# Optimization experiments

Measured on AMD Instinct MI355X. Metric: run time of the kernel, lower is better.

## Reference

```python
import jax, jax.numpy as jnp
import numpy as np

B, S = 256, 512
V, E, H, O = 256, 128, 256, 128


def setup_inputs() -> dict:
    key = jax.random.key(0)
    ks = jax.random.split(key, 8)
    s_e = 1.0 / np.sqrt(H)
    return {
        "x": jax.random.randint(ks[0], (B, S), 0, V),
        "emb": jax.random.normal(ks[1], (V, E), dtype=jnp.float32),
        "W_ih": jax.random.uniform(ks[2], (4 * H, E), jnp.float32, -s_e, s_e),
        "W_hh": jax.random.uniform(ks[3], (4 * H, H), jnp.float32, -s_e, s_e),
        "b_ih": jax.random.uniform(ks[4], (4 * H,), jnp.float32, -s_e, s_e),
        "b_hh": jax.random.uniform(ks[5], (4 * H,), jnp.float32, -s_e, s_e),
        "W_out": jax.random.uniform(ks[6], (O, H), jnp.float32, -s_e, s_e),
        "b_out": jax.random.uniform(ks[7], (O,), jnp.float32, -s_e, s_e),
    }


def _lstm_last_h(xe, W_ih, W_hh, b_ih, b_hh):
    # xe: [B, S, E]. Precompute input contribution to all gates: [S, B, 4H]
    pre = jnp.einsum("bse,ge->sbg", xe, W_ih) + (b_ih + b_hh)
    Bn = xe.shape[0]
    h0 = jnp.zeros((Bn, H), xe.dtype)
    c0 = jnp.zeros((Bn, H), xe.dtype)

    def step(carry, p):
        h, c = carry
        gates = p + h @ W_hh.T  # [B, 4H]
        i, f, g, o = jnp.split(gates, 4, axis=-1)  # PyTorch gate order i,f,g,o
        i = jax.nn.sigmoid(i)
        f = jax.nn.sigmoid(f)
        g = jnp.tanh(g)
        o = jax.nn.sigmoid(o)
        c = f * c + i * g
        h = o * jnp.tanh(c)
        return (h, c), None

    (h, _), _ = jax.lax.scan(step, (h0, c0), pre)
    return h  # [B, H] == lstm output at last timestep


def reference(x, emb, W_ih, W_hh, b_ih, b_hh, W_out, b_out):
    xe = emb[x]  # [B, S, E] embedding lookup
    h_last = _lstm_last_h(xe, W_ih, W_hh, b_ih, b_hh)
    return h_last @ W_out.T + b_out  # [B, O]
```

## Files before the change

kernel.cpp:

```cpp
#include <hip/hip_runtime.h>


typedef _Float16 f16x8 __attribute__((ext_vector_type(8)));
typedef _Float16 f16x4 __attribute__((ext_vector_type(4)));
typedef float    f32x4 __attribute__((ext_vector_type(4)));

#define B_  256
#define S_  512
#define V_  256
#define E_  128
#define H_  256
#define O_  128

#define T_OFF     0u
#define HLAST_OFF (512u << 10)
#define WPK_OFF   (768u << 10)

__global__ void build_table(const float* __restrict__ emb,
                            const float* __restrict__ W_ih,
                            const float* __restrict__ b_ih,
                            const float* __restrict__ b_hh,
                            _Float16* __restrict__ T2h) {
    const int v   = blockIdx.x;
    const int tid = threadIdx.x;

    __shared__ float e[E_];
    if (tid < E_) e[tid] = emb[v * E_ + tid];
    __syncthreads();

    f16x4 tv;
#pragma unroll
    for (int t = 0; t < 4; ++t) {
        const int g = t * 256 + tid;
        const float4* wp = (const float4*)(W_ih + g * E_);
        float acc = 0.f;
#pragma unroll
        for (int i = 0; i < E_ / 4; ++i) {
            float4 w = wp[i];
            acc += w.x * e[4*i] + w.y * e[4*i+1] + w.z * e[4*i+2] + w.w * e[4*i+3];
        }
        tv[t] = (_Float16)(acc + b_ih[g] + b_hh[g]);
    }
    *(f16x4*)(T2h + ((size_t)v * 256 + tid) * 4) = tv;
}

__global__ void prepack(const float* __restrict__ W_hh,
                        _Float16* __restrict__ Wpk) {
    const int blk = blockIdx.x;
    const int ktS = blk >> 3;
    const int j   = blk & 7;
    const int kt  = 3 + ktS * 4;
    const int tid = threadIdx.x;
    const int wv = tid >> 6, l = tid & 63, l15 = l & 15, quad = l >> 4;
    const int n  = j * 128 + wv * 16 + l15;
    const int k0 = kt * 32 + quad * 8;
    const float4* wp = (const float4*)(W_hh + (size_t)n * H_ + k0);
    float4 w0 = wp[0];
    float4 w1 = wp[1];
    f16x8 f = (f16x8){
        (_Float16)w0.x, (_Float16)w0.y, (_Float16)w0.z, (_Float16)w0.w,
        (_Float16)w1.x, (_Float16)w1.y, (_Float16)w1.z, (_Float16)w1.w};
    *(f16x8*)(Wpk + ((size_t)tid * 16 + blk) * 8) = f;
}

__device__ __forceinline__ float sig_fast(float x) {
    float t = __builtin_amdgcn_exp2f(-1.4426950408889634f * x);
    return __builtin_amdgcn_rcpf(1.f + t);
}
__device__ __forceinline__ float tanh_fast(float x) {
    x = fminf(fmaxf(x, -30.f), 30.f);
    float t = __builtin_amdgcn_exp2f(-2.8853900817779268f * x);
    return (1.f - t) * __builtin_amdgcn_rcpf(1.f + t);
}

#define HSTRIDE 272

__launch_bounds__(512, 2)
__global__ void lstm_persistent(const int* __restrict__ x,
                                const float* __restrict__ W_hh,
                                const _Float16* __restrict__ T2h,
                                const _Float16* __restrict__ Wpk,
                                float* __restrict__ hlast) {
    const int tid    = threadIdx.x;
    const int wv     = tid >> 6;
    const int l      = tid & 63;
    const int l15    = l & 15;
    const int quad   = l >> 4;
    const int stripe = blockIdx.x;
    const int uu     = wv * 16 + l15;

    __shared__ __align__(16) _Float16 wlds[8][8][2][512];
    __shared__ __align__(16) _Float16 hbuf[2][4][HSTRIDE];
    __shared__ __align__(16) _Float16 zbuf[256];

    if (tid < 128) ((int*)zbuf)[tid] = 0;

    f16x8 wreg[8][4];
#pragma unroll
    for (int j = 0; j < 8; ++j) {
        const float* wr = W_hh + (size_t)(j * 128 + uu) * H_ + quad * 8;
#pragma unroll
        for (int kt = 0; kt < 7; ++kt) {
            if (kt == 3) continue;
            const float4* wp = (const float4*)(wr + kt * 32);
            float4 w0 = wp[0];
            float4 w1 = wp[1];
            f16x8 f = (f16x8){
                (_Float16)w0.x, (_Float16)w0.y, (_Float16)w0.z, (_Float16)w0.w,
                (_Float16)w1.x, (_Float16)w1.y, (_Float16)w1.z, (_Float16)w1.w};
            if (kt < 2)
                *(f16x8*)&wlds[wv][j][kt][(size_t)l * 8] = f;
            else
                wreg[j][(kt == 2) ? 0 : kt - 3] = f;
        }
    }

    const int grow = stripe * 4 + quad;
    float c2[2] = {0.f, 0.f};

    const int* xp = x + (size_t)grow * S_;
    int xv = xp[0];

    f16x8 wstr[8];
    const _Float16* wpk_lane = Wpk + (size_t)tid * 128;

    const f32x4 z4 = (f32x4){0.f, 0.f, 0.f, 0.f};

    __syncthreads();

    for (int s = 0; s < S_; ++s) {
        f16x4 tcv[2];
        tcv[0] = *(const f16x4*)(T2h + ((size_t)xv * 256 + uu) * 4);
        tcv[1] = *(const f16x4*)(T2h + ((size_t)xv * 256 + uu + 128) * 4);
        if (s + 1 < S_) xv = xp[s + 1];

        f32x4 acc[8];

        if (s > 0) {
            const _Float16* ha = ((l15 & 3) == 0)
                ? (&hbuf[(s - 1) & 1][l15 >> 2][0] + quad * 8)
                : (zbuf + quad * 8);

            {
                f16x8 a = *(const f16x8*)(ha + 0 * 32);
#pragma unroll
                for (int j = 0; j < 8; ++j) {
                    f16x8 b = *(const f16x8*)&wlds[wv][j][0][(size_t)l * 8];
                    acc[j] = __builtin_amdgcn_mfma_f32_16x16x32_f16(
                        a, b, z4, 0, 0, 0);
                }
            }
            {
                f16x8 a = *(const f16x8*)(ha + 1 * 32);
#pragma unroll
                for (int j = 0; j < 8; ++j) {
                    f16x8 b = *(const f16x8*)&wlds[wv][j][1][(size_t)l * 8];
                    acc[j] = __builtin_amdgcn_mfma_f32_16x16x32_f16(
                        a, b, acc[j], 0, 0, 0);
                }
            }
            {
                f16x8 a = *(const f16x8*)(ha + 2 * 32);
#pragma unroll
                for (int j = 0; j < 8; ++j)
                    acc[j] = __builtin_amdgcn_mfma_f32_16x16x32_f16(
                        a, wreg[j][0], acc[j], 0, 0, 0);
            }
            {
                f16x8 a = *(const f16x8*)(ha + 3 * 32);
#pragma unroll
                for (int j = 0; j < 8; ++j)
                    acc[j] = __builtin_amdgcn_mfma_f32_16x16x32_f16(
                        a, wstr[j], acc[j], 0, 0, 0);
            }

            __builtin_amdgcn_sched_barrier(0);
#pragma unroll
            for (int j = 0; j < 8; ++j)
                wstr[j] = *(const f16x8*)(wpk_lane + 64 + j * 8);

#pragma unroll
            for (int m = 1; m < 4; ++m) {
                f16x8 a = *(const f16x8*)(ha + (m + 3) * 32);
#pragma unroll
                for (int j = 0; j < 8; ++j)
                    acc[j] = __builtin_amdgcn_mfma_f32_16x16x32_f16(
                        a, wreg[j][m], acc[j], 0, 0, 0);
            }
            {
                f16x8 a = *(const f16x8*)(ha + 7 * 32);
#pragma unroll
                for (int j = 0; j < 8; ++j)
                    acc[j] = __builtin_amdgcn_mfma_f32_16x16x32_f16(
                        a, wstr[j], acc[j], 0, 0, 0);
            }
        } else {
#pragma unroll
            for (int j = 0; j < 8; ++j) acc[j] = z4;
        }

        const bool last = (s == S_ - 1);
#pragma unroll
        for (int p = 0; p < 2; ++p) {
            float gi = sig_fast (acc[0 + p][0] + (float)tcv[p][0]);
            float gf = sig_fast (acc[2 + p][0] + (float)tcv[p][1]);
            float gg = tanh_fast(acc[4 + p][0] + (float)tcv[p][2]);
            float go = sig_fast (acc[6 + p][0] + (float)tcv[p][3]);
            float cc = gf * c2[p] + gi * gg;
            c2[p] = cc;
            float hv = go * tanh_fast(cc);
            if (!last) {
                hbuf[s & 1][quad][uu + p * 128] = (_Float16)hv;
            } else {
                hlast[(size_t)grow * H_ + uu + p * 128] = hv;
            }
        }

        if (!last) {
#pragma unroll
            for (int j = 0; j < 8; ++j)
                wstr[j] = *(const f16x8*)(wpk_lane + j * 8);
        }

        asm volatile("s_waitcnt lgkmcnt(0)" ::: "memory");
        __builtin_amdgcn_s_barrier();
    }
}

__global__ void out_kernel(const float* __restrict__ hlast,
                           const float* __restrict__ W_out,
                           const float* __restrict__ b_out,
                           float* __restrict__ out) {
    const int b = blockIdx.x;
    const int o = threadIdx.x;
    __shared__ float hl[H_];
    hl[o]       = hlast[b * H_ + o];
    hl[o + 128] = hlast[b * H_ + o + 128];
    __syncthreads();
    const float4* wp = (const float4*)(W_out + o * H_);
    float acc = 0.f;
#pragma unroll
    for (int i = 0; i < H_ / 4; ++i) {
        float4 w = wp[i];
        acc += w.x * hl[4*i] + w.y * hl[4*i+1] + w.z * hl[4*i+2] + w.w * hl[4*i+3];
    }
    out[b * O_ + o] = acc + b_out[o];
}

extern "C" void kernel_launch(void* const* d_in, const int* in_sizes, int n_in,
                              void* d_out, int out_size, void* d_ws, size_t ws_size,
                              hipStream_t stream) {
    const int*   x     = (const int*)  d_in[0];
    const float* emb   = (const float*)d_in[1];
    const float* W_ih  = (const float*)d_in[2];
    const float* W_hh  = (const float*)d_in[3];
    const float* b_ih  = (const float*)d_in[4];
    const float* b_hh  = (const float*)d_in[5];
    const float* W_out = (const float*)d_in[6];
    const float* b_out = (const float*)d_in[7];
    float* out = (float*)d_out;

    char* ws = (char*)d_ws;
    _Float16* T2h   = (_Float16*)(ws + T_OFF);
    float*    hlast = (float*)(ws + HLAST_OFF);
    _Float16* Wpk   = (_Float16*)(ws + WPK_OFF);

    build_table<<<dim3(V_), dim3(256), 0, stream>>>(emb, W_ih, b_ih, b_hh, T2h);
    prepack<<<dim3(16), dim3(512), 0, stream>>>(W_hh, Wpk);
    lstm_persistent<<<dim3(64), dim3(512), 0, stream>>>(x, W_hh, T2h, Wpk, hlast);
    out_kernel<<<dim3(B_), dim3(O_), 0, stream>>>(hlast, W_out, b_out, out);
}
```

Before: 866.1 us.

## Software-pipeline LSTM recurrence so half of hidden units overlap next step's MFMAs

Restructures the recurrent loop so only the first half of the hidden units is computed before the barrier. The second half's gate activations and cell update are interleaved with the first K-chunks of the next step's MFMA matmul, which consumes only the first half of h. A second barrier is inserted before the K-chunks that read the second half. Gate-table loads for the next token are prefetched one step earlier. The aim is to hide the serial activation latency behind matrix work, at the cost of an extra barrier per step and more live registers.

```diff
diff --git a/kernel.cpp b/kernel.cpp
--- a/kernel.cpp
+++ b/kernel.cpp
@@ -119,111 +119,134 @@
     float c2[2] = {0.f, 0.f};
 
     const int* xp = x + (size_t)grow * S_;
-    int xv = xp[0];
+    const f32x4 z4 = (f32x4){0.f, 0.f, 0.f, 0.f};
+
+    f32x4 acc[8];
+#pragma unroll
+    for (int j = 0; j < 8; ++j) acc[j] = z4;
+
+    f16x4 tcv[2];
+    tcv[0] = *(const f16x4*)(T2h + ((size_t)xp[0] * 256 + uu) * 4);
+    tcv[1] = *(const f16x4*)(T2h + ((size_t)xp[0] * 256 + uu + 128) * 4);
+    int xnext = xp[1];
 
     f16x8 wstr[8];
     const _Float16* wpk_lane = Wpk + (size_t)tid * 128;
-
-    const f32x4 z4 = (f32x4){0.f, 0.f, 0.f, 0.f};
+#pragma unroll
+    for (int j = 0; j < 8; ++j)
+        wstr[j] = *(const f16x8*)(wpk_lane + j * 8);
 
     __syncthreads();
 
     for (int s = 0; s < S_; ++s) {
-        f16x4 tcv[2];
-        tcv[0] = *(const f16x4*)(T2h + ((size_t)xv * 256 + uu) * 4);
-        tcv[1] = *(const f16x4*)(T2h + ((size_t)xv * 256 + uu + 128) * 4);
-        if (s + 1 < S_) xv = xp[s + 1];
-
-        f32x4 acc[8];
-
-        if (s > 0) {
-            const _Float16* ha = ((l15 & 3) == 0)
-                ? (&hbuf[(s - 1) & 1][l15 >> 2][0] + quad * 8)
-                : (zbuf + quad * 8);
-
-            {
-                f16x8 a = *(const f16x8*)(ha + 0 * 32);
-#pragma unroll
-                for (int j = 0; j < 8; ++j) {
-                    f16x8 b = *(const f16x8*)&wlds[wv][j][0][(size_t)l * 8];
-                    acc[j] = __builtin_amdgcn_mfma_f32_16x16x32_f16(
-                        a, b, z4, 0, 0, 0);
-                }
-            }
-            {
-                f16x8 a = *(const f16x8*)(ha + 1 * 32);
-#pragma unroll
-                for (int j = 0; j < 8; ++j) {
-                    f16x8 b = *(const f16x8*)&wlds[wv][j][1][(size_t)l * 8];
-                    acc[j] = __builtin_amdgcn_mfma_f32_16x16x32_f16(
-                        a, b, acc[j], 0, 0, 0);
-                }
-            }
-            {
-                f16x8 a = *(const f16x8*)(ha + 2 * 32);
-#pragma unroll
-                for (int j = 0; j < 8; ++j)
-                    acc[j] = __builtin_amdgcn_mfma_f32_16x16x32_f16(
-                        a, wreg[j][0], acc[j], 0, 0, 0);
-            }
-            {
-                f16x8 a = *(const f16x8*)(ha + 3 * 32);
-#pragma unroll
-                for (int j = 0; j < 8; ++j)
-                    acc[j] = __builtin_amdgcn_mfma_f32_16x16x32_f16(
-                        a, wstr[j], acc[j], 0, 0, 0);
-            }
-
-            __builtin_amdgcn_sched_barrier(0);
-#pragma unroll
-            for (int j = 0; j < 8; ++j)
-                wstr[j] = *(const f16x8*)(wpk_lane + 64 + j * 8);
-
-#pragma unroll
-            for (int m = 1; m < 4; ++m) {
-                f16x8 a = *(const f16x8*)(ha + (m + 3) * 32);
-#pragma unroll
-                for (int j = 0; j < 8; ++j)
-                    acc[j] = __builtin_amdgcn_mfma_f32_16x16x32_f16(
-                        a, wreg[j][m], acc[j], 0, 0, 0);
-            }
-            {
-                f16x8 a = *(const f16x8*)(ha + 7 * 32);
-#pragma unroll
-                for (int j = 0; j < 8; ++j)
-                    acc[j] = __builtin_amdgcn_mfma_f32_16x16x32_f16(
-                        a, wstr[j], acc[j], 0, 0, 0);
-            }
-        } else {
-#pragma unroll
-            for (int j = 0; j < 8; ++j) acc[j] = z4;
-        }
-
         const bool last = (s == S_ - 1);
-#pragma unroll
-        for (int p = 0; p < 2; ++p) {
-            float gi = sig_fast (acc[0 + p][0] + (float)tcv[p][0]);
-            float gf = sig_fast (acc[2 + p][0] + (float)tcv[p][1]);
-            float gg = tanh_fast(acc[4 + p][0] + (float)tcv[p][2]);
-            float go = sig_fast (acc[6 + p][0] + (float)tcv[p][3]);
-            float cc = gf * c2[p] + gi * gg;
-            c2[p] = cc;
+
+        float g1[4] = {acc[1][0], acc[3][0], acc[5][0], acc[7][0]};
+        {
+            float gi = sig_fast (acc[0][0] + (float)tcv[0][0]);
+            float gf = sig_fast (acc[2][0] + (float)tcv[0][1]);
+            float gg = tanh_fast(acc[4][0] + (float)tcv[0][2]);
+            float go = sig_fast (acc[6][0] + (float)tcv[0][3]);
+            float cc = gf * c2[0] + gi * gg;
+            c2[0] = cc;
             float hv = go * tanh_fast(cc);
-            if (!last) {
-                hbuf[s & 1][quad][uu + p * 128] = (_Float16)hv;
-            } else {
-                hlast[(size_t)grow * H_ + uu + p * 128] = hv;
-            }
-        }
-
-        if (!last) {
-#pragma unroll
-            for (int j = 0; j < 8; ++j)
-                wstr[j] = *(const f16x8*)(wpk_lane + j * 8);
+            if (!last) hbuf[s & 1][quad][uu] = (_Float16)hv;
+            else       hlast[(size_t)grow * H_ + uu] = hv;
+        }
+
+        if (last) {
+            float gi = sig_fast (g1[0] + (float)tcv[1][0]);
+            float gf = sig_fast (g1[1] + (float)tcv[1][1]);
+            float gg = tanh_fast(g1[2] + (float)tcv[1][2]);
+            float go = sig_fast (g1[3] + (float)tcv[1][3]);
+            float cc = gf * c2[1] + gi * gg;
+            float hv = go * tanh_fast(cc);
+            hlast[(size_t)grow * H_ + uu + 128] = hv;
+            break;
         }
 
         asm volatile("s_waitcnt lgkmcnt(0)" ::: "memory");
         __builtin_amdgcn_s_barrier();
+
+        f16x4 tn0 = *(const f16x4*)(T2h + ((size_t)xnext * 256 + uu) * 4);
+        f16x4 tn1 = *(const f16x4*)(T2h + ((size_t)xnext * 256 + uu + 128) * 4);
+        if (s + 2 < S_) xnext = xp[s + 2];
+
+        const _Float16* ha = ((l15 & 3) == 0)
+            ? (&hbuf[s & 1][l15 >> 2][0] + quad * 8)
+            : (zbuf + quad * 8);
+
+        {
+            f16x8 a = *(const f16x8*)(ha + 0 * 32);
+#pragma unroll
+            for (int j = 0; j < 8; ++j) {
+                f16x8 b = *(const f16x8*)&wlds[wv][j][0][(size_t)l * 8];
+                acc[j] = __builtin_amdgcn_mfma_f32_16x16x32_f16(
+                    a, b, z4, 0, 0, 0);
+            }
+        }
+        float gi1 = sig_fast(g1[0] + (float)tcv[1][0]);
+        float gf1 = sig_fast(g1[1] + (float)tcv[1][1]);
+        {
+            f16x8 a = *(const f16x8*)(ha + 1 * 32);
+#pragma unroll
+            for (int j = 0; j < 8; ++j) {
+                f16x8 b = *(const f16x8*)&wlds[wv][j][1][(size_t)l * 8];
+                acc[j] = __builtin_amdgcn_mfma_f32_16x16x32_f16(
+                    a, b, acc[j], 0, 0, 0);
+            }
+        }
+        float gg1 = tanh_fast(g1[2] + (float)tcv[1][2]);
+        float go1 = sig_fast (g1[3] + (float)tcv[1][3]);
+        {
+            f16x8 a = *(const f16x8*)(ha + 2 * 32);
+#pragma unroll
+            for (int j = 0; j < 8; ++j)
+                acc[j] = __builtin_amdgcn_mfma_f32_16x16x32_f16(
+                    a, wreg[j][0], acc[j], 0, 0, 0);
+        }
+        float cc1 = gf1 * c2[1] + gi1 * gg1;
+        c2[1] = cc1;
+        float hv1 = go1 * tanh_fast(cc1);
+        {
+            f16x8 a = *(const f16x8*)(ha + 3 * 32);
+#pragma unroll
+            for (int j = 0; j < 8; ++j)
+                acc[j] = __builtin_amdgcn_mfma_f32_16x16x32_f16(
+                    a, wstr[j], acc[j], 0, 0, 0);
+        }
+        hbuf[s & 1][quad][uu + 128] = (_Float16)hv1;
+
+        __builtin_amdgcn_sched_barrier(0);
+#pragma unroll
+        for (int j = 0; j < 8; ++j)
+            wstr[j] = *(const f16x8*)(wpk_lane + 64 + j * 8);
+
+        asm volatile("s_waitcnt lgkmcnt(0)" ::: "memory");
+        __builtin_amdgcn_s_barrier();
+
+#pragma unroll
+        for (int m = 1; m < 4; ++m) {
+            f16x8 a = *(const f16x8*)(ha + (m + 3) * 32);
+#pragma unroll
+            for (int j = 0; j < 8; ++j)
+                acc[j] = __builtin_amdgcn_mfma_f32_16x16x32_f16(
+                    a, wreg[j][m], acc[j], 0, 0, 0);
+        }
+        {
+            f16x8 a = *(const f16x8*)(ha + 7 * 32);
+#pragma unroll
+            for (int j = 0; j < 8; ++j)
+                acc[j] = __builtin_amdgcn_mfma_f32_16x16x32_f16(
+                    a, wstr[j], acc[j], 0, 0, 0);
+        }
+
+#pragma unroll
+        for (int j = 0; j < 8; ++j)
+            wstr[j] = *(const f16x8*)(wpk_lane + j * 8);
+
+        tcv[0] = tn0;
+        tcv[1] = tn1;
     }
 }
 
```

Result: slower. 1.985 ms (+129.2%).
